# Optimization experiments

Hardware: AMD Instinct MI355X
Metric: run time of the kernel (lower is better)

Reference implementation:

```python
import math
import jax, jax.numpy as jnp
from jax import lax
import numpy as np

DN = ('NCHW', 'OIHW', 'NCHW')


def setup_inputs() -> dict:
    key = jax.random.key(0)
    k0, k1, k2, k3, k4, k5 = jax.random.split(key, 6)
    n, c, h, w = 16, 256, 64, 64
    x = jax.random.normal(k0, (n, c, h, w), jnp.float32)
    b1 = math.sqrt(3.0 / h)
    p1 = jax.random.uniform(k1, (h, c // 8), jnp.float32, -b1, b1)          # p_1_w
    p3 = jax.random.normal(k2, (c, 1, 9, 9), jnp.float32) * 0.05            # depthwise conv, groups=c
    p4 = jax.random.normal(k3, (c, 4, 5, 1), jnp.float32) * 0.05            # grouped conv, groups=c//4
    b5 = math.sqrt(3.0 / (c * w // 8))
    p5 = jax.random.uniform(k4, (c // 8, w, 1, 3 * c), jnp.float32, -b5, b5)  # p_5_w
    p6 = jax.random.normal(k5, (c, 1, 1, 3), jnp.float32) * 0.3             # depthwise conv, groups=c
    return {"x": x, "p1": p1, "p3": p3, "p4": p4, "p5": p5, "p6": p6}


def reference(x, p1, p3, p4, p5, p6):
    n, c, h, w = x.shape
    # t_1: einsum 'abcd,ce->abed' contracts h -> (n, c, c//8, w)
    t1 = jnp.einsum('nchw,he->ncew', x, p1)
    # t_2: unfold(x, (3,1), padding=(1,0)) -> (n, c, 3, h, w)
    xp = jnp.pad(x, ((0, 0), (0, 0), (1, 1), (0, 0)))
    t2 = jnp.stack([xp[:, :, k:k + h, :] for k in range(3)], axis=2)
    # p_3: 9x9 depthwise conv over the (c//8, w) 'spatial' map
    t3 = lax.conv_general_dilated(t1, p3, (1, 1), ((4, 4), (4, 4)),
                                  dimension_numbers=DN, feature_group_count=c)
    # p_4: (5,1) conv with groups=c//4
    t4 = lax.conv_general_dilated(t3, p4, (1, 1), ((2, 2), (0, 0)),
                                  dimension_numbers=DN, feature_group_count=c // 4)
    # t_5: einsum 'abcd,cdef->abef' -> (n, c, 1, 3c) -> (n, c, 3c)
    t5 = jnp.einsum('ncew,ewf->ncf', t4, p5[:, :, 0, :])
    # p_6: (1,3) depthwise conv on (n, c, 1, 3c)
    t6 = lax.conv_general_dilated(t5[:, :, None, :], p6, (1, 1), ((0, 0), (1, 1)),
                                  dimension_numbers=DN, feature_group_count=c)[:, :, 0, :]
    # scaled bmm: (n,c,3c) @ (n,3c,h*w) / sqrt(3c)
    out = jnp.einsum('ncf,nfp->ncp', t6, t2.reshape(n, 3 * c, h * w))
    return (out / math.sqrt(3 * c)).reshape(n, c, h, w)
```

## Files before the change

### kernel.cpp

```cpp
#include <hip/hip_runtime.h>

#define NB 16
#define C  256
#define H  64
#define W  64
#define E  32
#define F  768
#define HW 4096
#define K5 2048
#define XROWS 4224

typedef __attribute__((ext_vector_type(4))) float f32x4;
typedef __attribute__((ext_vector_type(16))) float f32x16;
typedef __attribute__((ext_vector_type(8))) short s16x8;

__device__ inline unsigned short to_bf16(float f) {
  union { float f; unsigned u; } v; v.f = f;
  unsigned u = v.u;
  u += 0x7fff + ((u >> 16) & 1);
  return (unsigned short)(u >> 16);
}

__device__ inline float from_bf16(unsigned short s) {
  union { unsigned u; float f; } v; v.u = ((unsigned)s) << 16;
  return v.f;
}

__device__ inline void gload16(const void* g, void* l) {
  __builtin_amdgcn_global_load_lds((const __attribute__((address_space(1))) unsigned int*)g,
                                   (__attribute__((address_space(3))) unsigned int*)l, 16, 0, 0);
}

__global__ __launch_bounds__(256) void k_t13(const float* __restrict__ x,
                                             const float* __restrict__ p1,
                                             const float* __restrict__ p3,
                                             unsigned short* __restrict__ t3g) {
  const int nc = blockIdx.x;
  const int c = nc & 255;
  const int tid = threadIdx.x;
  __shared__ __align__(16) float p1t[32][68];
  __shared__ __align__(16) float t1s[40][76];
  for (int i = tid; i < 40 * 76; i += 256) (&t1s[0][0])[i] = 0.f;
  for (int i = tid; i < 2048; i += 256) {
    int h = i >> 5, e = i & 31;
    p1t[e][h] = p1[i];
  }
  __syncthreads();
  {
    const int w = tid & 63;
    const int e0 = tid >> 6;
    const float* xp = x + (size_t)nc * HW;
    float acc[8] = {0.f, 0.f, 0.f, 0.f, 0.f, 0.f, 0.f, 0.f};
#pragma unroll
    for (int hb = 0; hb < 4; ++hb) {
      float xv[16];
#pragma unroll
      for (int j = 0; j < 16; ++j) xv[j] = xp[(hb * 16 + j) * 64 + w];
#pragma unroll
      for (int i = 0; i < 8; ++i) {
        const float* pr = &p1t[e0 + 4 * i][hb * 16];
#pragma unroll
        for (int jb = 0; jb < 4; ++jb) {
          float4 pv = *(const float4*)(pr + jb * 4);
          acc[i] += xv[jb * 4 + 0] * pv.x + xv[jb * 4 + 1] * pv.y +
                    xv[jb * 4 + 2] * pv.z + xv[jb * 4 + 3] * pv.w;
        }
      }
    }
#pragma unroll
    for (int i = 0; i < 8; ++i) t1s[4 + e0 + 4 * i][4 + w] = acc[i];
  }
  __syncthreads();
  unsigned short* plane = t3g + (size_t)nc * 2304;
  if (tid < 32) {
    static const int zr[4] = {0, 1, 34, 35};
    int row = zr[tid >> 3], col = (tid & 7) * 8;
    uint4 z = make_uint4(0, 0, 0, 0);
    *(uint4*)(plane + row * 64 + col) = z;
  }
  const int e = tid >> 3, w0 = (tid & 7) * 8;
  const float* w3 = p3 + c * 81;
  float o[8];
#pragma unroll
  for (int k = 0; k < 8; ++k) o[k] = 0.f;
#pragma unroll
  for (int i = 0; i < 9; ++i) {
    float win[16];
    const float* r = &t1s[e + i][w0];
    *(float4*)&win[0]  = *(const float4*)(r);
    *(float4*)&win[4]  = *(const float4*)(r + 4);
    *(float4*)&win[8]  = *(const float4*)(r + 8);
    *(float4*)&win[12] = *(const float4*)(r + 12);
#pragma unroll
    for (int j = 0; j < 9; ++j) {
      float wt = w3[i * 9 + j];
#pragma unroll
      for (int k = 0; k < 8; ++k) o[k] += win[j + k] * wt;
    }
  }
  unsigned short ob[8];
#pragma unroll
  for (int k = 0; k < 8; ++k) ob[k] = to_bf16(o[k]);
  *(uint4*)(plane + (2 + e) * 64 + w0) = *(const uint4*)ob;
}

__global__ __launch_bounds__(256) void k_t4k(const unsigned short* __restrict__ t3g,
                                             const float* __restrict__ p4,
                                             unsigned short* __restrict__ t4b) {
  const int nc = blockIdx.x;
  const int c = nc & 255;
  const int tid = threadIdx.x;
  const int e = tid >> 3, w0 = (tid & 7) * 8;
  const float* w4 = p4 + c * 20;
  float acc[8];
#pragma unroll
  for (int k = 0; k < 8; ++k) acc[k] = 0.f;
#pragma unroll
  for (int ci = 0; ci < 4; ++ci) {
    const unsigned short* plane = t3g + (size_t)((nc & ~3) + ci) * 2304;
#pragma unroll
    for (int u = 0; u < 5; ++u) {
      uint4 v = *(const uint4*)(plane + (e + u) * 64 + w0);
      const unsigned short* vs = (const unsigned short*)&v;
      float wv = w4[ci * 5 + u];
#pragma unroll
      for (int k = 0; k < 8; ++k) acc[k] += from_bf16(vs[k]) * wv;
    }
  }
  unsigned short ob[8];
#pragma unroll
  for (int k = 0; k < 8; ++k) ob[k] = to_bf16(acc[k]);
  *(uint4*)(t4b + (size_t)nc * 2048 + e * 64 + w0) = *(const uint4*)ob;
}

__global__ __launch_bounds__(256) void k_p5t(const float* __restrict__ p5,
                                             unsigned short* __restrict__ p5t) {
  const int f0 = blockIdx.x * 64;
  const int k0 = blockIdx.y * 64;
  const int tid = threadIdx.x;
  __shared__ __align__(16) unsigned short ls[64][264];
  int fl = tid & 63, k4 = tid >> 6;
  for (int i = 0; i < 16; ++i) {
    int kl = k4 * 16 + i;
    ls[fl][kl] = to_bf16(p5[(size_t)(k0 + kl) * F + f0 + fl]);
  }
  __syncthreads();
#pragma unroll
  for (int j = 0; j < 2; ++j) {
    int chunk = tid + 256 * j;
    int row = chunk >> 3, slot = chunk & 7;
    *(uint4*)(p5t + (size_t)(f0 + row) * K5 + k0 + slot * 8) = *(const uint4*)&ls[row][slot * 8];
  }
}

__global__ __launch_bounds__(256) void k_xt(const float* __restrict__ x,
                                            unsigned short* __restrict__ xt) {
  const int hi = blockIdx.x;
  const int n = blockIdx.y;
  const int tid = threadIdx.x;
  unsigned short* dst = xt + ((size_t)n * XROWS + hi * 64) * C;
  if (hi == 0 || hi == 65) {
    uint4 z = make_uint4(0, 0, 0, 0);
    uint4* d4 = (uint4*)dst;
#pragma unroll
    for (int i = 0; i < 8; ++i) d4[tid + 256 * i] = z;
    return;
  }
  const int h = hi - 1;
  __shared__ __align__(16) unsigned short ls[64][264];
  const float* xp = x + ((size_t)n * C) * HW + h * 64;
  int w = tid & 63, c4 = tid >> 6;
  for (int i = 0; i < 64; ++i) {
    int c = c4 * 64 + i;
    ls[w][c] = to_bf16(xp[(size_t)c * HW + w]);
  }
  __syncthreads();
#pragma unroll
  for (int j = 0; j < 8; ++j) {
    int chunk = tid + 256 * j;
    int row = chunk >> 5, slot = chunk & 31;
    *(uint4*)(dst + row * C + slot * 8) = *(const uint4*)&ls[row][slot * 8];
  }
}

__global__ __launch_bounds__(256) void k_t5m(const unsigned short* __restrict__ A,
                                             const unsigned short* __restrict__ Bt,
                                             unsigned short* __restrict__ Cout) {
  const int bid = blockIdx.x;
  const int wg = (bid & 7) * 96 + (bid >> 3);
  const int nt = wg % 12;
  const int mt = wg / 12;
  const int n0 = nt * 64;
  const int m0 = mt * 64;
  const int tid = threadIdx.x;
  const int lane = tid & 63;
  const int wave = tid >> 6;
  const int wm = wave >> 1, wn = wave & 1;
  __shared__ __align__(16) short As[8192];
  __shared__ __align__(16) short Bs[8192];
  f32x16 acc = {};

  for (int k0 = 0; k0 < K5; k0 += 128) {
#pragma unroll
    for (int i = 0; i < 4; ++i) {
      int chunk = i * 256 + tid;
      int r = chunk >> 4, sl = chunk & 15;
      int sw = sl ^ (r & 15);
      gload16((const char*)(A + (size_t)(m0 + r) * K5 + k0) + sw * 16,
              (char*)As + chunk * 16);
      gload16((const char*)(Bt + (size_t)(n0 + r) * K5 + k0) + sw * 16,
              (char*)Bs + chunk * 16);
    }
    __syncthreads();
#pragma unroll
    for (int kq = 0; kq < 8; ++kq) {
      int arow = wm * 32 + (lane & 31);
      int aslot = (kq * 2 + (lane >> 5)) ^ (arow & 15);
      s16x8 af = *(const s16x8*)((const char*)As + arow * 256 + aslot * 16);
      int brow = wn * 32 + (lane & 31);
      int bslot = (kq * 2 + (lane >> 5)) ^ (brow & 15);
      s16x8 bf = *(const s16x8*)((const char*)Bs + brow * 256 + bslot * 16);
      acc = __builtin_amdgcn_mfma_f32_32x32x16_bf16(af, bf, acc, 0, 0, 0);
    }
    __syncthreads();
  }
  const int col = n0 + wn * 32 + (lane & 31);
#pragma unroll
  for (int r = 0; r < 16; ++r) {
    int grow = m0 + wm * 32 + (r & 3) + 8 * (r >> 2) + 4 * (lane >> 5);
    Cout[(size_t)grow * F + col] = to_bf16(acc[r]);
  }
}

__global__ __launch_bounds__(256) void k_t6(const unsigned short* __restrict__ t5b,
                                            const float* __restrict__ p6,
                                            unsigned short* __restrict__ t6b) {
  int idx = blockIdx.x * 256 + threadIdx.x;
  if (idx >= NB * C * F) return;
  int fp = idx % F;
  int nc = idx / F;
  int c = nc & 255;
  int c2 = fp & 255;
  int kk = fp >> 8;
  int f = 3 * c2 + kk;
  const unsigned short* row = t5b + (size_t)nc * F;
  const float* wt = p6 + c * 3;
  float acc = from_bf16(row[f]) * wt[1];
  if (f > 0) acc += from_bf16(row[f - 1]) * wt[0];
  if (f < F - 1) acc += from_bf16(row[f + 1]) * wt[2];
  t6b[idx] = to_bf16(acc * 0.03608439182435161f);
}

__global__ __launch_bounds__(512, 4) void k_outm(const unsigned short* __restrict__ t6b,
                                                 const unsigned short* __restrict__ xt,
                                                 float* __restrict__ outp) {
  const int bid = blockIdx.x;
  const int wg = (bid & 7) * 64 + (bid >> 3);
  const int n  = wg >> 5;
  const int tile = wg & 31;
  const int p0 = (tile & 15) * 256;
  const int m0 = (tile >> 4) * 128;
  const int tid = threadIdx.x;
  const int lane = tid & 63;
  const int wid = tid >> 6;
  const int wm = wid >> 2;
  const int wn = wid & 3;
  __shared__ __align__(16) short As[8192];
  __shared__ __align__(16) short Bs[16384];
  f32x16 acc[2][2] = {};
  const unsigned short* Abase = t6b + (size_t)(n * C) * F + m0 * F;
  const unsigned short* Xbase = xt + (size_t)n * XROWS * C;

  for (int kt = 0; kt < 12; ++kt) {
    const int k0 = kt * 64;
    const int kk = k0 >> 8, c20 = k0 & 255;
#pragma unroll
    for (int i = 0; i < 2; ++i) {
      int chunk = i * 512 + tid;
      int r = chunk >> 3, sl = chunk & 7, sw = sl ^ (r & 7);
      gload16((const char*)(Abase + (size_t)r * F + k0) + sw * 16,
              (char*)As + chunk * 16);
    }
#pragma unroll
    for (int i = 0; i < 4; ++i) {
      int chunk = i * 512 + tid;
      int r = chunk >> 3, sl = chunk & 7, sw = sl ^ (r & 7);
      gload16((const char*)(Xbase + (size_t)(p0 + r + (kk << 6)) * C + c20) + sw * 16,
              (char*)Bs + chunk * 16);
    }
    __syncthreads();
#pragma unroll
    for (int kq = 0; kq < 4; ++kq) {
      s16x8 af[2], bf[2];
#pragma unroll
      for (int mi = 0; mi < 2; ++mi) {
        int row = wm * 64 + mi * 32 + (lane & 31);
        int byte = (row * 128 + kq * 32 + ((lane >> 5) * 16)) ^ ((row & 7) << 4);
        af[mi] = *(const s16x8*)((const char*)As + byte);
      }
#pragma unroll
      for (int ni = 0; ni < 2; ++ni) {
        int row = wn * 64 + ni * 32 + (lane & 31);
        int byte = (row * 128 + kq * 32 + ((lane >> 5) * 16)) ^ ((row & 7) << 4);
        bf[ni] = *(const s16x8*)((const char*)Bs + byte);
      }
#pragma unroll
      for (int mi = 0; mi < 2; ++mi)
#pragma unroll
        for (int ni = 0; ni < 2; ++ni)
          acc[mi][ni] = __builtin_amdgcn_mfma_f32_32x32x16_bf16(af[mi], bf[ni], acc[mi][ni], 0, 0, 0);
    }
    __syncthreads();
  }
  float* obase = outp + ((size_t)(n * C) + m0) * HW;
#pragma unroll
  for (int mi = 0; mi < 2; ++mi) {
#pragma unroll
    for (int ni = 0; ni < 2; ++ni) {
      int gcol = p0 + wn * 64 + ni * 32 + (lane & 31);
#pragma unroll
      for (int r = 0; r < 16; ++r) {
        int grow = wm * 64 + mi * 32 + (r & 3) + 8 * (r >> 2) + 4 * (lane >> 5);
        obase[(size_t)grow * HW + gcol] = acc[mi][ni][r];
      }
    }
  }
}

extern "C" void kernel_launch(void* const* d_in, const int* in_sizes, int n_in,
                              void* d_out, int out_size, void* d_ws, size_t ws_size,
                              hipStream_t stream) {
  (void)in_sizes; (void)n_in; (void)out_size; (void)ws_size;
  const float* x  = (const float*)d_in[0];
  const float* p1 = (const float*)d_in[1];
  const float* p3 = (const float*)d_in[2];
  const float* p4 = (const float*)d_in[3];
  const float* p5 = (const float*)d_in[4];
  const float* p6 = (const float*)d_in[5];
  float* out = (float*)d_out;

  char* ws = (char*)d_ws;
  unsigned short* t3g = (unsigned short*)ws;
  unsigned short* t4b = (unsigned short*)(ws + 18874368);
  unsigned short* p5t = (unsigned short*)(ws + 35651584);
  unsigned short* t5b = (unsigned short*)(ws + 38797312);
  unsigned short* t6b = (unsigned short*)ws;
  unsigned short* xt  = (unsigned short*)(ws + 6291456);

  k_t13<<<dim3(NB * C), 256, 0, stream>>>(x, p1, p3, t3g);
  k_t4k<<<dim3(NB * C), 256, 0, stream>>>(t3g, p4, t4b);
  k_p5t<<<dim3(12, 32), 256, 0, stream>>>(p5, p5t);
  k_t5m<<<dim3(768), 256, 0, stream>>>(t4b, p5t, t5b);
  k_t6 <<<dim3((NB * C * F + 255) / 256), 256, 0, stream>>>(t5b, p6, t6b);
  k_xt <<<dim3(66, NB), 256, 0, stream>>>(x, xt);
  k_outm<<<dim3(512), 512, 0, stream>>>(t6b, xt, out);
}
```

Measured before the change: 147.8 us.

## Use bf16 MFMA for h-contraction and packed-FMA depthwise conv in t13

```diff
diff --git a/kernel.cpp b/kernel.cpp
--- a/kernel.cpp
+++ b/kernel.cpp
@@ -10,6 +10,7 @@
 #define K5 2048
 #define XROWS 4224
 
+typedef __attribute__((ext_vector_type(2))) float f32x2;
 typedef __attribute__((ext_vector_type(4))) float f32x4;
 typedef __attribute__((ext_vector_type(16))) float f32x16;
 typedef __attribute__((ext_vector_type(8))) short s16x8;
@@ -31,44 +32,88 @@
                                    (__attribute__((address_space(3))) unsigned int*)l, 16, 0, 0);
 }
 
+__global__ __launch_bounds__(192) void k_wp(const float* __restrict__ p3,
+                                            float* __restrict__ w3p) {
+  const int c = blockIdx.x;
+  const int t = threadIdx.x;
+  if (t >= 180) return;
+  const int i = t / 20, s = t % 20;
+  const float* wr = p3 + c * 81 + i * 9;
+  float v;
+  if (s < 10) {
+    int q = s >> 1, e = s & 1;
+    v = (q < 4) ? wr[2 * q + e] : (e ? 0.f : wr[8]);
+  } else {
+    int s2 = s - 10, q = s2 >> 1, e = s2 & 1;
+    v = (q == 0) ? (e ? wr[0] : 0.f) : wr[2 * (q - 1) + 1 + e];
+  }
+  w3p[(size_t)(c * 9 + i) * 20 + s] = v;
+}
+
 __global__ __launch_bounds__(256) void k_t13(const float* __restrict__ x,
                                              const float* __restrict__ p1,
-                                             const float* __restrict__ p3,
+                                             const float* __restrict__ w3p,
                                              unsigned short* __restrict__ t3g) {
   const int nc = blockIdx.x;
   const int c = nc & 255;
   const int tid = threadIdx.x;
-  __shared__ __align__(16) float p1t[32][68];
+  const int lane = tid & 63;
+  const int wv = tid >> 6;
+
+  __shared__ __align__(16) unsigned short xs[64][64];
   __shared__ __align__(16) float t1s[40][76];
+
   for (int i = tid; i < 40 * 76; i += 256) (&t1s[0][0])[i] = 0.f;
-  for (int i = tid; i < 2048; i += 256) {
-    int h = i >> 5, e = i & 31;
-    p1t[e][h] = p1[i];
+
+  s16x8 afr[2][2];
+  {
+    const int r = lane & 15;
+    const int kb = (lane >> 4) * 8;
+#pragma unroll
+    for (int m = 0; m < 2; ++m)
+#pragma unroll
+      for (int kc = 0; kc < 2; ++kc) {
+        s16x8 tmp;
+#pragma unroll
+        for (int j = 0; j < 8; ++j)
+          tmp[j] = (short)to_bf16(p1[(kc * 32 + kb + j) * 32 + m * 16 + r]);
+        afr[m][kc] = tmp;
+      }
+  }
+  {
+    const float* xp = x + (size_t)nc * HW;
+#pragma unroll
+    for (int t = 0; t < 2; ++t) {
+      int uid = tid + 256 * t;
+      int h = uid >> 3, uc = uid & 7;
+      float4 v0 = *(const float4*)(xp + h * 64 + uc * 8);
+      float4 v1 = *(const float4*)(xp + h * 64 + uc * 8 + 4);
+      unsigned short b[8] = {to_bf16(v0.x), to_bf16(v0.y), to_bf16(v0.z), to_bf16(v0.w),
+                             to_bf16(v1.x), to_bf16(v1.y), to_bf16(v1.z), to_bf16(v1.w)};
+      *(uint4*)((char*)&xs[0][0] + h * 128 + ((uc ^ ((h >> 3) & 7)) * 16)) = *(const uint4*)b;
+    }
   }
   __syncthreads();
   {
-    const int w = tid & 63;
-    const int e0 = tid >> 6;
-    const float* xp = x + (size_t)nc * HW;
-    float acc[8] = {0.f, 0.f, 0.f, 0.f, 0.f, 0.f, 0.f, 0.f};
-#pragma unroll
-    for (int hb = 0; hb < 4; ++hb) {
-      float xv[16];
-#pragma unroll
-      for (int j = 0; j < 16; ++j) xv[j] = xp[(hb * 16 + j) * 64 + w];
-#pragma unroll
-      for (int i = 0; i < 8; ++i) {
-        const float* pr = &p1t[e0 + 4 * i][hb * 16];
-#pragma unroll
-        for (int jb = 0; jb < 4; ++jb) {
-          float4 pv = *(const float4*)(pr + jb * 4);
-          acc[i] += xv[jb * 4 + 0] * pv.x + xv[jb * 4 + 1] * pv.y +
-                    xv[jb * 4 + 2] * pv.z + xv[jb * 4 + 3] * pv.w;
-        }
-      }
-    }
-#pragma unroll
-    for (int i = 0; i < 8; ++i) t1s[4 + e0 + 4 * i][4 + w] = acc[i];
+    const int wcol = wv * 16 + (lane & 15);
+    f32x4 cf[2] = {{0.f, 0.f, 0.f, 0.f}, {0.f, 0.f, 0.f, 0.f}};
+#pragma unroll
+    for (int kc = 0; kc < 2; ++kc) {
+      const int kb = kc * 32 + (lane >> 4) * 8;
+      const char* base = (const char*)&xs[0][0] +
+                         kb * 128 + (((wcol >> 3) ^ ((kb >> 3) & 7)) * 16) + (wcol & 7) * 2;
+      s16x8 bfrag;
+#pragma unroll
+      for (int j = 0; j < 8; ++j)
+        bfrag[j] = *(const short*)(base + j * 128);
+      cf[0] = __builtin_amdgcn_mfma_f32_16x16x32_bf16(afr[0][kc], bfrag, cf[0], 0, 0, 0);
+      cf[1] = __builtin_amdgcn_mfma_f32_16x16x32_bf16(afr[1][kc], bfrag, cf[1], 0, 0, 0);
+    }
+#pragma unroll
+    for (int m = 0; m < 2; ++m)
+#pragma unroll
+      for (int q = 0; q < 4; ++q)
+        t1s[4 + m * 16 + (lane >> 4) * 4 + q][4 + wcol] = cf[m][q];
   }
   __syncthreads();
   unsigned short* plane = t3g + (size_t)nc * 2304;
@@ -79,28 +124,46 @@
     *(uint4*)(plane + row * 64 + col) = z;
   }
   const int e = tid >> 3, w0 = (tid & 7) * 8;
-  const float* w3 = p3 + c * 81;
-  float o[8];
-#pragma unroll
-  for (int k = 0; k < 8; ++k) o[k] = 0.f;
+  f32x2 opk[8] = {};
 #pragma unroll
   for (int i = 0; i < 9; ++i) {
-    float win[16];
     const float* r = &t1s[e + i][w0];
-    *(float4*)&win[0]  = *(const float4*)(r);
-    *(float4*)&win[4]  = *(const float4*)(r + 4);
-    *(float4*)&win[8]  = *(const float4*)(r + 8);
-    *(float4*)&win[12] = *(const float4*)(r + 12);
-#pragma unroll
-    for (int j = 0; j < 9; ++j) {
-      float wt = w3[i * 9 + j];
-#pragma unroll
-      for (int k = 0; k < 8; ++k) o[k] += win[j + k] * wt;
+    f32x4 v0 = *(const f32x4*)(r);
+    f32x4 v1 = *(const f32x4*)(r + 4);
+    f32x4 v2 = *(const f32x4*)(r + 8);
+    f32x4 v3 = *(const f32x4*)(r + 12);
+    f32x2 wa[8];
+    wa[0] = __builtin_shufflevector(v0, v0, 0, 1);
+    wa[1] = __builtin_shufflevector(v0, v0, 2, 3);
+    wa[2] = __builtin_shufflevector(v1, v1, 0, 1);
+    wa[3] = __builtin_shufflevector(v1, v1, 2, 3);
+    wa[4] = __builtin_shufflevector(v2, v2, 0, 1);
+    wa[5] = __builtin_shufflevector(v2, v2, 2, 3);
+    wa[6] = __builtin_shufflevector(v3, v3, 0, 1);
+    wa[7] = __builtin_shufflevector(v3, v3, 2, 3);
+    const f32x2* wp = (const f32x2*)(w3p + (size_t)(c * 9 + i) * 20);
+    f32x2 we0 = wp[0], we1 = wp[1], we2 = wp[2], we3 = wp[3], we4 = wp[4];
+    f32x2 wo0 = wp[5], wo1 = wp[6], wo2 = wp[7], wo3 = wp[8], wo4 = wp[9];
+#pragma unroll
+    for (int t = 0; t < 4; ++t) {
+      f32x2 aE = opk[2 * t], aO = opk[2 * t + 1];
+      aE += wa[t] * we0;
+      aE += wa[t + 1] * we1;
+      aE += wa[t + 2] * we2;
+      aE += wa[t + 3] * we3;
+      aE += wa[t + 4] * we4;
+      aO += wa[t] * wo0;
+      aO += wa[t + 1] * wo1;
+      aO += wa[t + 2] * wo2;
+      aO += wa[t + 3] * wo3;
+      aO += wa[t + 4] * wo4;
+      opk[2 * t] = aE;
+      opk[2 * t + 1] = aO;
     }
   }
   unsigned short ob[8];
 #pragma unroll
-  for (int k = 0; k < 8; ++k) ob[k] = to_bf16(o[k]);
+  for (int k = 0; k < 8; ++k) ob[k] = to_bf16(opk[k].x + opk[k].y);
   *(uint4*)(plane + (2 + e) * 64 + w0) = *(const uint4*)ob;
 }
 
@@ -344,10 +407,12 @@
   unsigned short* t4b = (unsigned short*)(ws + 18874368);
   unsigned short* p5t = (unsigned short*)(ws + 35651584);
   unsigned short* t5b = (unsigned short*)(ws + 38797312);
+  float*          w3p = (float*)(ws + 47290368);
   unsigned short* t6b = (unsigned short*)ws;
   unsigned short* xt  = (unsigned short*)(ws + 6291456);
 
-  k_t13<<<dim3(NB * C), 256, 0, stream>>>(x, p1, p3, t3g);
+  k_wp <<<dim3(C), 192, 0, stream>>>(p3, w3p);
+  k_t13<<<dim3(NB * C), 256, 0, stream>>>(x, p1, w3p, t3g);
   k_t4k<<<dim3(NB * C), 256, 0, stream>>>(t3g, p4, t4b);
   k_p5t<<<dim3(12, 32), 256, 0, stream>>>(p5, p5t);
   k_t5m<<<dim3(768), 256, 0, stream>>>(t4b, p5t, t5b);
```

New measurement: 133.6 us. 1.11x faster.
